# Kernel optimization log

Measured on AMD Instinct MI355X. Metric: run time of the kernel, lower is better.

Reference implementation:

```python
import math
import jax, jax.numpy as jnp
import numpy as np

DIM = 2048
NUM_HEADS = 16
HEAD_DIM = 128
SEQ = 2048
BATCH = 2
HIDDEN = 5632  # round_up(int(4*2048*2/3), 256)
EPS = 1e-6


def setup_inputs() -> dict:
    key = jax.random.key(0)
    ks = jax.random.split(key, 8)
    s = 0.02
    x = jax.random.normal(ks[0], (BATCH, SEQ, DIM), jnp.float32)
    wq = jax.random.normal(ks[1], (DIM, NUM_HEADS * HEAD_DIM), jnp.float32) * s
    wk = jax.random.normal(ks[2], (DIM, NUM_HEADS * HEAD_DIM), jnp.float32) * s
    wv = jax.random.normal(ks[3], (DIM, NUM_HEADS * HEAD_DIM), jnp.float32) * s
    wo = jax.random.normal(ks[4], (NUM_HEADS * HEAD_DIM, DIM), jnp.float32) * s
    w_mlp = jax.random.normal(ks[5], (HIDDEN, DIM), jnp.float32) * s
    v_mlp = jax.random.normal(ks[6], (HIDDEN, DIM), jnp.float32) * s
    w2_mlp = jax.random.normal(ks[7], (DIM, HIDDEN), jnp.float32) * s
    norm1_w = jnp.ones((DIM,), jnp.float32)
    norm2_w = jnp.ones((DIM,), jnp.float32)
    # RoPE tables: theta_i = 10000^{-2i/head_dim}, angle[p,i] = p * theta_i
    inv_freq = 1.0 / (10000.0 ** (np.arange(0, HEAD_DIM, 2, dtype=np.float32) / HEAD_DIM))
    angles = np.arange(SEQ, dtype=np.float32)[:, None] * inv_freq[None, :]  # [S, D/2]
    freqs_cos = jnp.asarray(np.cos(angles))
    freqs_sin = jnp.asarray(np.sin(angles))
    return {"x": x, "wq": wq, "wk": wk, "wv": wv, "wo": wo,
            "w_mlp": w_mlp, "v_mlp": v_mlp, "w2_mlp": w2_mlp,
            "norm1_w": norm1_w, "norm2_w": norm2_w,
            "freqs_cos": freqs_cos, "freqs_sin": freqs_sin}


def _rope(t, cos, sin):
    # t: [B,S,H,D] -> pairs, complex multiply by (cos + i sin)
    B, S, H, D = t.shape
    t = t.reshape(B, S, H, D // 2, 2)
    x0, x1 = t[..., 0], t[..., 1]
    c = cos[None, :S, None, :]
    s = sin[None, :S, None, :]
    o0 = x0 * c - x1 * s
    o1 = x0 * s + x1 * c
    return jnp.stack([o0, o1], axis=-1).reshape(B, S, H, D)


def _rmsnorm(x, w):
    x = x * jax.lax.rsqrt(jnp.mean(x * x, axis=-1, keepdims=True) + EPS)
    return w * x


def _attention(x, wq, wk, wv, wo, cos, sin):
    B, S, _ = x.shape
    q = (x @ wq).reshape(B, S, NUM_HEADS, HEAD_DIM)
    k = (x @ wk).reshape(B, S, NUM_HEADS, HEAD_DIM)
    v = (x @ wv).reshape(B, S, NUM_HEADS, HEAD_DIM)
    q = _rope(q, cos, sin)
    k = _rope(k, cos, sin)
    scores = jnp.einsum('bqhd,bkhd->bhqk', q, k) / math.sqrt(HEAD_DIM)
    causal = jnp.tril(jnp.ones((S, S), bool))
    scores = jnp.where(causal[None, None], scores, -jnp.inf)
    probs = jax.nn.softmax(scores.astype(jnp.float32), axis=-1)
    o = jnp.einsum('bhqk,bkhd->bqhd', probs, v).reshape(B, S, NUM_HEADS * HEAD_DIM)
    return o @ wo


def _mlp(x, w, v, w2):
    return (jax.nn.silu(x @ w.T) * (x @ v.T)) @ w2.T


def reference(x, wq, wk, wv, wo, w_mlp, v_mlp, w2_mlp, norm1_w, norm2_w, freqs_cos, freqs_sin):
    x = x + _attention(x, wq, wk, wv, wo, freqs_cos, freqs_sin)
    x = _rmsnorm(x, norm1_w)
    x = x + _mlp(x, w_mlp, v_mlp, w2_mlp)
    x = _rmsnorm(x, norm2_w)
    return x
```

## Files before the change

kernel.cpp:

```cpp
#include <hip/hip_runtime.h>

typedef unsigned short u16;
typedef unsigned int u32;
typedef float f32x4 __attribute__((ext_vector_type(4)));
typedef short bf16x8 __attribute__((ext_vector_type(8)));

#define DIM 2048
#define SEQ 2048
#define NHEAD 16
#define HDIM 128
#define BATCH 2
#define HIDDEN 5632
#define ROWS 4096

__device__ __forceinline__ float b2f(u16 h) { return __uint_as_float(((u32)h) << 16); }
__device__ __forceinline__ u16 f2b(float f) {
  u32 u = __float_as_uint(f);
  return (u16)((u + 0x7fffu + ((u >> 16) & 1u)) >> 16);
}

__global__ __launch_bounds__(256) void cvt_f2b(const float* __restrict__ in, u16* __restrict__ out, int n) {
  int i = (blockIdx.x * 256 + threadIdx.x) * 4;
  if (i < n) {
    float4 v = *(const float4*)(in + i);
    u32 p0 = (u32)f2b(v.x) | ((u32)f2b(v.y) << 16);
    u32 p1 = (u32)f2b(v.z) | ((u32)f2b(v.w) << 16);
    *(uint2*)(out + i) = make_uint2(p0, p1);
  }
}

__global__ __launch_bounds__(256) void cvtT(const float* __restrict__ in, u16* __restrict__ out,
                                            int Rr, int Cc) {
  __shared__ float t[32][33];
  int tx = threadIdx.x & 31, ty = threadIdx.x >> 5;
  int r0 = blockIdx.y * 32, c0 = blockIdx.x * 32;
#pragma unroll
  for (int rr = 0; rr < 4; ++rr)
    t[ty + rr * 8][tx] = in[(size_t)(r0 + ty + rr * 8) * Cc + c0 + tx];
  __syncthreads();
#pragma unroll
  for (int rr = 0; rr < 4; ++rr)
    out[(size_t)(c0 + ty + rr * 8) * Rr + r0 + tx] = f2b(t[tx][ty + rr * 8]);
}

__device__ __forceinline__ void stage_tile(u16* lds, const u16* __restrict__ g,
                                           int row0, int col0, int ld, int wave, int lane) {
#pragma unroll
  for (int j = 0; j < 2; ++j) {
    int i = wave * 2 + j;
    const u16* gp = g + (size_t)(row0 + i * 16 + (lane >> 2)) * ld + col0 + (lane & 3) * 8;
    __builtin_amdgcn_global_load_lds((const __attribute__((address_space(1))) void*)gp,
                                     (__attribute__((address_space(3))) void*)(lds + i * 512),
                                     16, 0, 0);
  }
}

template <int EPI>
__global__ __launch_bounds__(256) void gemm_bt(const u16* __restrict__ A, const u16* __restrict__ Bt,
                                               const void* R_, void* C_, int M, int N, int K) {
  __shared__ u16 lA[2][4096];
  __shared__ u16 lB[2][4096];
  const int tid = threadIdx.x, lane = tid & 63, wave = tid >> 6;
  const int wm = wave >> 1, wn = wave & 1;
  const int gx = gridDim.x;
  const int nwg = gx * gridDim.y;
  const int id = blockIdx.y * gx + blockIdx.x;
  const int cpx = nwg >> 3;
  const int sw = (id & 7) * cpx + (id >> 3);
  const int m0 = (sw / gx) * 128, n0 = (sw % gx) * 128;
  const int rl = lane & 15, g = lane >> 4;

  stage_tile(lA[0], A, m0, 0, K, wave, lane);
  stage_tile(lB[0], Bt, n0, 0, K, wave, lane);

  f32x4 acc[4][4];
#pragma unroll
  for (int a = 0; a < 4; ++a)
#pragma unroll
    for (int b = 0; b < 4; ++b) acc[a][b] = (f32x4){0.f, 0.f, 0.f, 0.f};

  __syncthreads();

  const int nk = K / 32;
  for (int kt = 0; kt < nk; ++kt) {
    const int cur = kt & 1;
    if (kt + 1 < nk) {
      stage_tile(lA[cur ^ 1], A, m0, (kt + 1) * 32, K, wave, lane);
      stage_tile(lB[cur ^ 1], Bt, n0, (kt + 1) * 32, K, wave, lane);
    }
    bf16x8 af[4], bfr[4];
#pragma unroll
    for (int mi = 0; mi < 4; ++mi)
      af[mi] = *reinterpret_cast<const bf16x8*>(&lA[cur][(wm * 64 + mi * 16 + rl) * 32 + g * 8]);
#pragma unroll
    for (int ni = 0; ni < 4; ++ni)
      bfr[ni] = *reinterpret_cast<const bf16x8*>(&lB[cur][(wn * 64 + ni * 16 + rl) * 32 + g * 8]);
#pragma unroll
    for (int mi = 0; mi < 4; ++mi)
#pragma unroll
      for (int ni = 0; ni < 4; ++ni)
        acc[mi][ni] = __builtin_amdgcn_mfma_f32_16x16x32_bf16(af[mi], bfr[ni], acc[mi][ni], 0, 0, 0);
    __syncthreads();
  }

#pragma unroll
  for (int mi = 0; mi < 4; ++mi)
#pragma unroll
    for (int ni = 0; ni < 4; ++ni)
#pragma unroll
      for (int j = 0; j < 4; ++j) {
        size_t row = m0 + wm * 64 + mi * 16 + g * 4 + j;
        size_t col = n0 + wn * 64 + ni * 16 + rl;
        size_t idx = row * N + col;
        float v = acc[mi][ni][j];
        if (EPI == 0) {
          ((u16*)C_)[idx] = f2b(v);
        } else if (EPI == 1) {
          ((float*)C_)[idx] = v + ((const float*)R_)[idx];
        } else if (EPI == 2) {
          float av = b2f(((const u16*)R_)[idx]);
          ((u16*)C_)[idx] = f2b(v * av / (1.f + __expf(-av)));
        } else if (EPI == 3) {
          ((float*)C_)[idx] = v + b2f(((const u16*)R_)[idx]);
        } else {
          size_t di = (col >> 11) * (size_t)(ROWS * (size_t)DIM) + row * DIM + (col & (DIM - 1));
          ((u16*)C_)[di] = f2b(v);
        }
      }
}

__global__ __launch_bounds__(256) void vtrans(const u16* __restrict__ V, u16* __restrict__ Vt) {
  __shared__ u16 t[32][33];
  int tx = threadIdx.x & 31, ty = threadIdx.x >> 5;
  int s0 = blockIdx.x * 32, d0 = blockIdx.y * 32;
  int bh = blockIdx.z, b = bh >> 4, h = bh & 15;
#pragma unroll
  for (int rr = 0; rr < 4; ++rr)
    t[ty + rr * 8][tx] = V[(size_t)(b * SEQ + s0 + ty + rr * 8) * DIM + h * HDIM + d0 + tx];
  __syncthreads();
#pragma unroll
  for (int rr = 0; rr < 4; ++rr)
    Vt[(size_t)(bh * HDIM + d0 + ty + rr * 8) * SEQ + s0 + tx] = t[tx][ty + rr * 8];
}

__global__ __launch_bounds__(256) void rope_kernel(u16* __restrict__ Q, u16* __restrict__ Kv,
                                                   const float* __restrict__ Cz, const float* __restrict__ Sz) {
  int t = blockIdx.x * 256 + threadIdx.x;
  int i = t & 63;
  int hh = (t >> 6) & 15;
  int row = t >> 10;
  int s = row & (SEQ - 1);
  float c = Cz[s * 64 + i], sn = Sz[s * 64 + i];
  size_t off = (size_t)row * DIM + hh * HDIM + 2 * i;
  const float sc = 0.08838834764831843f;

  u32 qp = *(const u32*)(Q + off);
  float q0 = b2f((u16)qp), q1 = b2f((u16)(qp >> 16));
  float o0 = (q0 * c - q1 * sn) * sc, o1 = (q0 * sn + q1 * c) * sc;
  *(u32*)(Q + off) = (u32)f2b(o0) | ((u32)f2b(o1) << 16);

  u32 kp = *(const u32*)(Kv + off);
  float k0 = b2f((u16)kp), k1 = b2f((u16)(kp >> 16));
  o0 = k0 * c - k1 * sn; o1 = k0 * sn + k1 * c;
  *(u32*)(Kv + off) = (u32)f2b(o0) | ((u32)f2b(o1) << 16);
}

__device__ __forceinline__ void attn_stage(u16* lk, u16* lv, const u16* __restrict__ Kg,
                                           const u16* __restrict__ Vg, int b, int h, int bh,
                                           int t, int w, int lane) {
  const int r4 = lane >> 2;
  const int gsw = (lane & 3) ^ (r4 & 3);
#pragma unroll
  for (int j = 0; j < 4; ++j) {
    const u16* gp = Kg + (size_t)(b * SEQ + t * 64 + j * 16 + r4) * DIM +
                    h * HDIM + w * 32 + gsw * 8;
    __builtin_amdgcn_global_load_lds((const __attribute__((address_space(1))) void*)gp,
                                     (__attribute__((address_space(3))) void*)(lk + w * 2048 + j * 512),
                                     16, 0, 0);
  }
#pragma unroll
  for (int j = 0; j < 4; ++j) {
    int id = w * 4 + j, kc2 = id >> 3, rg = id & 7;
    const u16* gp = Vg + (size_t)(bh * HDIM + rg * 16 + r4) * SEQ +
                    t * 64 + kc2 * 32 + gsw * 8;
    __builtin_amdgcn_global_load_lds((const __attribute__((address_space(1))) void*)gp,
                                     (__attribute__((address_space(3))) void*)(lv + kc2 * 4096 + rg * 512),
                                     16, 0, 0);
  }
}

__device__ __forceinline__ void attn_tile(const bf16x8* qf, float* m, float* l, f32x4* oacc,
                                          int qg0, int t, bool diag,
                                          const u16* lk, const u16* lv, u16 (*pl)[72],
                                          int rl, int g) {
  const int gx8 = (g ^ (rl & 3)) * 8;
  f32x4 s[4];
#pragma unroll
  for (int ct = 0; ct < 4; ++ct) s[ct] = (f32x4){0.f, 0.f, 0.f, 0.f};
#pragma unroll
  for (int ct = 0; ct < 4; ++ct)
#pragma unroll
    for (int kc = 0; kc < 4; ++kc) {
      bf16x8 kf = *reinterpret_cast<const bf16x8*>(&lk[kc * 2048 + (ct * 16 + rl) * 32 + gx8]);
      s[ct] = __builtin_amdgcn_mfma_f32_16x16x32_bf16(qf[kc], kf, s[ct], 0, 0, 0);
    }
  if (diag) {
#pragma unroll
    for (int ct = 0; ct < 4; ++ct) {
      int kg = t * 64 + ct * 16 + rl;
#pragma unroll
      for (int j = 0; j < 4; ++j)
        if (kg > qg0 + j) s[ct][j] = -1e30f;
    }
  }
  float mx[4], al[4];
#pragma unroll
  for (int j = 0; j < 4; ++j)
    mx[j] = fmaxf(fmaxf(s[0][j], s[1][j]), fmaxf(s[2][j], s[3][j]));
#pragma unroll
  for (int off = 1; off < 16; off <<= 1)
#pragma unroll
    for (int j = 0; j < 4; ++j) mx[j] = fmaxf(mx[j], __shfl_xor(mx[j], off));
#pragma unroll
  for (int j = 0; j < 4; ++j) {
    float mn = fmaxf(m[j], mx[j]);
    al[j] = __expf(m[j] - mn);
    m[j] = mn;
  }
  float rs[4] = {0.f, 0.f, 0.f, 0.f};
#pragma unroll
  for (int ct = 0; ct < 4; ++ct)
#pragma unroll
    for (int j = 0; j < 4; ++j) {
      float p = __expf(s[ct][j] - m[j]);
      s[ct][j] = p;
      rs[j] += p;
    }
#pragma unroll
  for (int off = 1; off < 16; off <<= 1)
#pragma unroll
    for (int j = 0; j < 4; ++j) rs[j] += __shfl_xor(rs[j], off);
#pragma unroll
  for (int j = 0; j < 4; ++j) l[j] = l[j] * al[j] + rs[j];
#pragma unroll
  for (int dt = 0; dt < 8; ++dt)
#pragma unroll
    for (int j = 0; j < 4; ++j) oacc[dt][j] *= al[j];

#pragma unroll
  for (int ct = 0; ct < 4; ++ct)
#pragma unroll
    for (int j = 0; j < 4; ++j) pl[g * 4 + j][ct * 16 + rl] = f2b(s[ct][j]);

  bf16x8 pa[2];
#pragma unroll
  for (int kc2 = 0; kc2 < 2; ++kc2)
    pa[kc2] = *reinterpret_cast<const bf16x8*>(&pl[rl][kc2 * 32 + g * 8]);

#pragma unroll
  for (int dt = 0; dt < 8; ++dt)
#pragma unroll
    for (int kc2 = 0; kc2 < 2; ++kc2) {
      bf16x8 vf = *reinterpret_cast<const bf16x8*>(&lv[kc2 * 4096 + (dt * 16 + rl) * 32 + gx8]);
      oacc[dt] = __builtin_amdgcn_mfma_f32_16x16x32_bf16(pa[kc2], vf, oacc[dt], 0, 0, 0);
    }
}

__global__ __launch_bounds__(256) void attn_kernel(const u16* __restrict__ Q, const u16* __restrict__ Kp,
                                                   const u16* __restrict__ Vt, u16* __restrict__ O) {
  const int lane = threadIdx.x & 63;
  const int w = threadIdx.x >> 6;
  const int id = blockIdx.y * 16 + blockIdx.x;
  const int sw = (id & 7) * 64 + (id >> 3);
  const int qa = sw & 15;
  const int qb = 31 - qa;
  const int bh = sw >> 4;
  const int b = bh >> 4, h = bh & 15;
  const int rl = lane & 15, g = lane >> 4;

  __shared__ u16 lK[2][8192];
  __shared__ u16 lV[2][8192];
  __shared__ u16 plds[4][16][72];

  const size_t qrowA = (size_t)b * SEQ + qa * 64 + w * 16;
  const size_t qrowB = (size_t)b * SEQ + qb * 64 + w * 16;
  bf16x8 qfA[4], qfB[4];
#pragma unroll
  for (int kc = 0; kc < 4; ++kc) {
    qfA[kc] = *reinterpret_cast<const bf16x8*>(Q + (qrowA + rl) * DIM + h * HDIM + kc * 32 + g * 8);
    qfB[kc] = *reinterpret_cast<const bf16x8*>(Q + (qrowB + rl) * DIM + h * HDIM + kc * 32 + g * 8);
  }

  float mA[4], lA_[4], mB[4], lB_[4];
  f32x4 oA[8], oB[8];
#pragma unroll
  for (int j = 0; j < 4; ++j) { mA[j] = -1e30f; lA_[j] = 0.f; mB[j] = -1e30f; lB_[j] = 0.f; }
#pragma unroll
  for (int dt = 0; dt < 8; ++dt) { oA[dt] = (f32x4){0.f, 0.f, 0.f, 0.f}; oB[dt] = (f32x4){0.f, 0.f, 0.f, 0.f}; }

  const int qg0A = qa * 64 + w * 16 + g * 4;
  const int qg0B = qb * 64 + w * 16 + g * 4;

  attn_stage(lK[0], lV[0], Kp, Vt, b, h, bh, 0, w, lane);

  int buf = 0;
  for (int t = 0; t <= qb; ++t) {
    if (t < qb) {
      attn_stage(lK[buf ^ 1], lV[buf ^ 1], Kp, Vt, b, h, bh, t + 1, w, lane);
      asm volatile("s_waitcnt vmcnt(8)" ::: "memory");
    } else {
      asm volatile("s_waitcnt vmcnt(0)" ::: "memory");
    }
    __builtin_amdgcn_s_barrier();
    __builtin_amdgcn_sched_barrier(0);
    attn_tile(qfB, mB, lB_, oB, qg0B, t, t == qb, lK[buf], lV[buf], plds[w], rl, g);
    if (t <= qa)
      attn_tile(qfA, mA, lA_, oA, qg0A, t, t == qa, lK[buf], lV[buf], plds[w], rl, g);
    asm volatile("s_waitcnt lgkmcnt(0)" ::: "memory");
    __builtin_amdgcn_sched_barrier(0);
    __builtin_amdgcn_s_barrier();
    buf ^= 1;
  }

  float invA[4], invB[4];
#pragma unroll
  for (int j = 0; j < 4; ++j) { invA[j] = 1.f / lA_[j]; invB[j] = 1.f / lB_[j]; }
#pragma unroll
  for (int dt = 0; dt < 8; ++dt)
#pragma unroll
    for (int j = 0; j < 4; ++j) {
      O[(qrowA + g * 4 + j) * DIM + h * HDIM + dt * 16 + rl] = f2b(oA[dt][j] * invA[j]);
      O[(qrowB + g * 4 + j) * DIM + h * HDIM + dt * 16 + rl] = f2b(oB[dt][j] * invB[j]);
    }
}

__global__ __launch_bounds__(256) void rmsnorm_to_bf16(const float* __restrict__ X, const float* __restrict__ W,
                                                       u16* __restrict__ O) {
  int row = blockIdx.x, tid = threadIdx.x;
  const float* xr = X + (size_t)row * DIM + tid * 8;
  float4 a = *(const float4*)xr;
  float4 bq = *(const float4*)(xr + 4);
  float v[8] = {a.x, a.y, a.z, a.w, bq.x, bq.y, bq.z, bq.w};
  float ss = 0.f;
#pragma unroll
  for (int j = 0; j < 8; ++j) ss += v[j] * v[j];
#pragma unroll
  for (int off = 32; off; off >>= 1) ss += __shfl_xor(ss, off);
  __shared__ float wss[4];
  int wave = tid >> 6, lane = tid & 63;
  if (lane == 0) wss[wave] = ss;
  __syncthreads();
  float r = rsqrtf((wss[0] + wss[1] + wss[2] + wss[3]) * (1.f / DIM) + 1e-6f);
  float4 wa = *(const float4*)(W + tid * 8);
  float4 wb = *(const float4*)(W + tid * 8 + 4);
  float wv[8] = {wa.x, wa.y, wa.z, wa.w, wb.x, wb.y, wb.z, wb.w};
  uint4 ou;
  ou.x = (u32)f2b(v[0] * r * wv[0]) | ((u32)f2b(v[1] * r * wv[1]) << 16);
  ou.y = (u32)f2b(v[2] * r * wv[2]) | ((u32)f2b(v[3] * r * wv[3]) << 16);
  ou.z = (u32)f2b(v[4] * r * wv[4]) | ((u32)f2b(v[5] * r * wv[5]) << 16);
  ou.w = (u32)f2b(v[6] * r * wv[6]) | ((u32)f2b(v[7] * r * wv[7]) << 16);
  *(uint4*)(O + (size_t)row * DIM + tid * 8) = ou;
}

__global__ __launch_bounds__(256) void rmsnorm_to_f32(const float* __restrict__ X, const float* __restrict__ W,
                                                      float* __restrict__ O) {
  int row = blockIdx.x, tid = threadIdx.x;
  const float* xr = X + (size_t)row * DIM + tid * 8;
  float4 a = *(const float4*)xr;
  float4 bq = *(const float4*)(xr + 4);
  float v[8] = {a.x, a.y, a.z, a.w, bq.x, bq.y, bq.z, bq.w};
  float ss = 0.f;
#pragma unroll
  for (int j = 0; j < 8; ++j) ss += v[j] * v[j];
#pragma unroll
  for (int off = 32; off; off >>= 1) ss += __shfl_xor(ss, off);
  __shared__ float wss[4];
  int wave = tid >> 6, lane = tid & 63;
  if (lane == 0) wss[wave] = ss;
  __syncthreads();
  float r = rsqrtf((wss[0] + wss[1] + wss[2] + wss[3]) * (1.f / DIM) + 1e-6f);
  float4 wa = *(const float4*)(W + tid * 8);
  float4 wb = *(const float4*)(W + tid * 8 + 4);
  float wv[8] = {wa.x, wa.y, wa.z, wa.w, wb.x, wb.y, wb.z, wb.w};
  float4 o0 = {v[0] * r * wv[0], v[1] * r * wv[1], v[2] * r * wv[2], v[3] * r * wv[3]};
  float4 o1 = {v[4] * r * wv[4], v[5] * r * wv[5], v[6] * r * wv[6], v[7] * r * wv[7]};
  *(float4*)(O + (size_t)row * DIM + tid * 8) = o0;
  *(float4*)(O + (size_t)row * DIM + tid * 8 + 4) = o1;
}

extern "C" void kernel_launch(void* const* d_in, const int* in_sizes, int n_in,
                              void* d_out, int out_size, void* d_ws, size_t ws_size,
                              hipStream_t stream) {
  const float* x     = (const float*)d_in[0];
  const float* wq    = (const float*)d_in[1];
  const float* wk    = (const float*)d_in[2];
  const float* wv    = (const float*)d_in[3];
  const float* wo    = (const float*)d_in[4];
  const float* w_mlp = (const float*)d_in[5];
  const float* v_mlp = (const float*)d_in[6];
  const float* w2    = (const float*)d_in[7];
  const float* n1w   = (const float*)d_in[8];
  const float* n2w   = (const float*)d_in[9];
  const float* fcos  = (const float*)d_in[10];
  const float* fsin  = (const float*)d_in[11];

  u16* ws = (u16*)d_ws;
  const size_t SZ = (size_t)ROWS * DIM;
  const size_t DD = (size_t)DIM * DIM;
  const size_t DH = (size_t)DIM * HIDDEN;

  u16* xb  = ws;
  u16* q   = ws + SZ;
  u16* k   = ws + 2 * SZ;
  u16* v   = ws + 3 * SZ;
  u16* vt  = ws + 4 * SZ;
  u16* hb  = ws + 5 * SZ;
  u16* W   = ws + 6 * SZ;
  u16* wqT = W;
  u16* wkT = W + DD;
  u16* wvT = W + 2 * DD;
  u16* woT = W + 3 * DD;
  u16* wmb = W;
  u16* vmb = W + DH;
  u16* w2b = W;
  float* x1f = (float*)ws;
  float* x2f = (float*)ws;
  u16* ba  = ws + 2 * SZ;

  dim3 blk(256);

  cvt_f2b<<<(int)(SZ / 4 / 256), blk, 0, stream>>>(x, xb, (int)SZ);
  dim3 gT(DIM / 32, DIM / 32);
  cvtT<<<gT, blk, 0, stream>>>(wq, wqT, DIM, DIM);
  cvtT<<<gT, blk, 0, stream>>>(wk, wkT, DIM, DIM);
  cvtT<<<gT, blk, 0, stream>>>(wv, wvT, DIM, DIM);
  cvtT<<<gT, blk, 0, stream>>>(wo, woT, DIM, DIM);

  dim3 gQKV(3 * DIM / 128, ROWS / 128);
  gemm_bt<4><<<gQKV, blk, 0, stream>>>(xb, W, nullptr, q, ROWS, 3 * DIM, DIM);

  cvt_f2b<<<(int)(DH / 4 / 256), blk, 0, stream>>>(w_mlp, wmb, (int)DH);

  rope_kernel<<<(ROWS * NHEAD * 64) / 256, blk, 0, stream>>>(q, k, fcos, fsin);
  vtrans<<<dim3(SEQ / 32, HDIM / 32, BATCH * NHEAD), blk, 0, stream>>>(v, vt);

  attn_kernel<<<dim3(16, BATCH * NHEAD), blk, 0, stream>>>(q, k, vt, v);

  dim3 gP(DIM / 128, ROWS / 128);
  gemm_bt<1><<<gP, blk, 0, stream>>>(v, woT, x, x1f, ROWS, DIM, DIM);

  cvt_f2b<<<(int)(DH / 4 / 256), blk, 0, stream>>>(v_mlp, vmb, (int)DH);

  rmsnorm_to_bf16<<<ROWS, blk, 0, stream>>>(x1f, n1w, hb);

  dim3 gM1(HIDDEN / 128, ROWS / 128);
  gemm_bt<0><<<gM1, blk, 0, stream>>>(hb, wmb, nullptr, ba, ROWS, HIDDEN, DIM);
  gemm_bt<2><<<gM1, blk, 0, stream>>>(hb, vmb, ba, ba, ROWS, HIDDEN, DIM);

  cvt_f2b<<<(int)(DH / 4 / 256), blk, 0, stream>>>(w2, w2b, (int)DH);

  gemm_bt<3><<<gP, blk, 0, stream>>>(ba, w2b, hb, x2f, ROWS, DIM, HIDDEN);
  rmsnorm_to_f32<<<ROWS, blk, 0, stream>>>(x2f, n2w, (float*)d_out);
}
```

Measured before the change: 842.7 us.

## Add 256x256 eight-wave pipelined GEMM for QKV and MLP up projections

Adds a new 512-thread GEMM kernel with 256x256 output tiles. It double-buffers LDS through direct global-to-LDS loads and interleaves the next tile's loads with MFMA phases, using explicit waitcnt, barriers and setprio. It also remaps block IDs in a swizzled order for L2 locality. The QKV and both MLP up-projection GEMMs now use it instead of the 128x128 kernel, aiming for more data reuse and better overlap of memory with compute. The cost is higher register and LDS pressure, and hand-tuned synchronization that is fragile.

```diff
diff --git a/kernel.cpp b/kernel.cpp
--- a/kernel.cpp
+++ b/kernel.cpp
@@ -129,6 +129,114 @@
       }
 }
 
+template <int EPI>
+__global__ __launch_bounds__(512, 2) void gemm8p(const u16* __restrict__ A, const u16* __restrict__ Bt,
+                                                 const void* R_, void* C_, int M, int N, int K) {
+  __shared__ u16 L[2][2][2][8192];
+  const int tid = threadIdx.x;
+  const int lane = tid & 63, wid = tid >> 6;
+  const int wr = wid >> 2, wc = wid & 3;
+  const int rl = lane & 15, g = lane >> 4;
+  const int s2 = ((rl >> 3) & 1) << 1;
+  const int gx = gridDim.x;
+  const int id = blockIdx.y * gx + blockIdx.x;
+  const int cpx = (gx * gridDim.y) >> 3;
+  const int sw = (id & 7) * cpx + (id >> 3);
+  const int m0 = (sw / gx) * 256, n0 = (sw % gx) * 256;
+  const int nk = K >> 6;
+
+  const int srow = tid >> 2;
+  const int sslot = (tid & 3) ^ (((tid >> 5) & 1) << 1);
+
+  auto SH = [&](int ks, int ab, int hf) {
+    const u16* src = ab ? Bt : A;
+    const u16* gp = src + (size_t)((ab ? n0 : m0) + hf * 128 + srow) * K + ks * 64 + sslot * 8;
+#pragma unroll
+    for (int kk = 0; kk < 2; ++kk)
+      __builtin_amdgcn_global_load_lds(
+          (const __attribute__((address_space(1))) void*)(gp + kk * 32),
+          (__attribute__((address_space(3))) void*)&L[ks & 1][ab][hf][kk * 4096 + wid * 512],
+          16, 0, 0);
+  };
+
+  f32x4 acc[8][4];
+#pragma unroll
+  for (int a = 0; a < 8; ++a)
+#pragma unroll
+    for (int b = 0; b < 4; ++b) acc[a][b] = (f32x4){0.f, 0.f, 0.f, 0.f};
+  bf16x8 bf[4][2];
+
+#define PHASE8(kst, q, STAGE, VMN)                                                              \
+  do {                                                                                          \
+    const int c_ = (kst) & 1;                                                                   \
+    if ((q) == 0) {                                                                             \
+      _Pragma("unroll") for (int ni = 0; ni < 4; ++ni)                                          \
+          _Pragma("unroll") for (int kk = 0; kk < 2; ++kk)                                      \
+              bf[ni][kk] = *(const bf16x8*)&L[c_][1][wc >> 1]                                   \
+                  [kk * 4096 + ((wc & 1) * 64 + ni * 16 + rl) * 32 + (g ^ s2) * 8];             \
+    }                                                                                           \
+    bf16x8 af[2][2];                                                                            \
+    _Pragma("unroll") for (int mm = 0; mm < 2; ++mm)                                            \
+        _Pragma("unroll") for (int kk = 0; kk < 2; ++kk)                                        \
+            af[mm][kk] = *(const bf16x8*)&L[c_][0][wr]                                          \
+                [kk * 4096 + (((q) * 2 + mm) * 16 + rl) * 32 + (g ^ s2) * 8];                   \
+    STAGE;                                                                                      \
+    __builtin_amdgcn_s_barrier();                                                               \
+    asm volatile("s_waitcnt lgkmcnt(0)" ::: "memory");                                          \
+    __builtin_amdgcn_sched_barrier(0);                                                          \
+    __builtin_amdgcn_s_setprio(1);                                                              \
+    _Pragma("unroll") for (int kk = 0; kk < 2; ++kk)                                            \
+        _Pragma("unroll") for (int mm = 0; mm < 2; ++mm)                                        \
+            _Pragma("unroll") for (int ni = 0; ni < 4; ++ni)                                    \
+                acc[(q) * 2 + mm][ni] = __builtin_amdgcn_mfma_f32_16x16x32_bf16(                \
+                    af[mm][kk], bf[ni][kk], acc[(q) * 2 + mm][ni], 0, 0, 0);                    \
+    __builtin_amdgcn_s_setprio(0);                                                              \
+    if ((VMN) == 4) asm volatile("s_waitcnt vmcnt(4)" ::: "memory");                            \
+    else if ((VMN) == 0) asm volatile("s_waitcnt vmcnt(0)" ::: "memory");                       \
+    __builtin_amdgcn_s_barrier();                                                               \
+  } while (0)
+
+  SH(0, 0, 0); SH(0, 0, 1); SH(0, 1, 0); SH(0, 1, 1); SH(1, 1, 0); SH(1, 1, 1);
+  asm volatile("s_waitcnt vmcnt(4)" ::: "memory");
+  __builtin_amdgcn_s_barrier();
+
+  const int nk2 = nk >> 1;
+  for (int i = 0; i < nk2; ++i) {
+    const int k0 = 2 * i, k1 = 2 * i + 1;
+    const bool st2 = (k0 + 2) < nk, st3 = (k0 + 3) < nk;
+    PHASE8(k0, 0, SH(k1, 0, 0), -1);
+    PHASE8(k0, 1, SH(k1, 0, 1), -1);
+    PHASE8(k0, 2, if (st2) SH(k0 + 2, 1, 0), -1);
+    PHASE8(k0, 3, if (st2) SH(k0 + 2, 1, 1), st2 ? 4 : 0);
+    PHASE8(k1, 0, if (st2) SH(k0 + 2, 0, 0), -1);
+    PHASE8(k1, 1, if (st2) SH(k0 + 2, 0, 1), -1);
+    PHASE8(k1, 2, if (st3) SH(k0 + 3, 1, 0), -1);
+    PHASE8(k1, 3, if (st3) SH(k0 + 3, 1, 1), st2 ? 4 : 0);
+  }
+#undef PHASE8
+
+#pragma unroll
+  for (int mi = 0; mi < 8; ++mi)
+#pragma unroll
+    for (int ni = 0; ni < 4; ++ni)
+#pragma unroll
+      for (int j = 0; j < 4; ++j) {
+        size_t row = m0 + wr * 128 + mi * 16 + g * 4 + j;
+        size_t col = n0 + wc * 64 + ni * 16 + rl;
+        size_t idx = row * N + col;
+        float v = acc[mi][ni][j];
+        if (EPI == 0) {
+          ((u16*)C_)[idx] = f2b(v);
+        } else if (EPI == 2) {
+          float av = b2f(((const u16*)R_)[idx]);
+          ((u16*)C_)[idx] = f2b(v * av / (1.f + __expf(-av)));
+        } else {
+          size_t di = (col >> 11) * (size_t)(ROWS * (size_t)DIM) + row * DIM + (col & (DIM - 1));
+          ((u16*)C_)[di] = f2b(v);
+        }
+      }
+}
+
 __global__ __launch_bounds__(256) void vtrans(const u16* __restrict__ V, u16* __restrict__ Vt) {
   __shared__ u16 t[32][33];
   int tx = threadIdx.x & 31, ty = threadIdx.x >> 5;
@@ -428,6 +536,7 @@
   u16* ba  = ws + 2 * SZ;
 
   dim3 blk(256);
+  dim3 blk8(512);
 
   cvt_f2b<<<(int)(SZ / 4 / 256), blk, 0, stream>>>(x, xb, (int)SZ);
   dim3 gT(DIM / 32, DIM / 32);
@@ -436,8 +545,8 @@
   cvtT<<<gT, blk, 0, stream>>>(wv, wvT, DIM, DIM);
   cvtT<<<gT, blk, 0, stream>>>(wo, woT, DIM, DIM);
 
-  dim3 gQKV(3 * DIM / 128, ROWS / 128);
-  gemm_bt<4><<<gQKV, blk, 0, stream>>>(xb, W, nullptr, q, ROWS, 3 * DIM, DIM);
+  dim3 gQKV(3 * DIM / 256, ROWS / 256);
+  gemm8p<4><<<gQKV, blk8, 0, stream>>>(xb, W, nullptr, q, ROWS, 3 * DIM, DIM);
 
   cvt_f2b<<<(int)(DH / 4 / 256), blk, 0, stream>>>(w_mlp, wmb, (int)DH);
 
@@ -453,9 +562,9 @@
 
   rmsnorm_to_bf16<<<ROWS, blk, 0, stream>>>(x1f, n1w, hb);
 
-  dim3 gM1(HIDDEN / 128, ROWS / 128);
-  gemm_bt<0><<<gM1, blk, 0, stream>>>(hb, wmb, nullptr, ba, ROWS, HIDDEN, DIM);
-  gemm_bt<2><<<gM1, blk, 0, stream>>>(hb, vmb, ba, ba, ROWS, HIDDEN, DIM);
+  dim3 gM8(HIDDEN / 256, ROWS / 256);
+  gemm8p<0><<<gM8, blk8, 0, stream>>>(hb, wmb, nullptr, ba, ROWS, HIDDEN, DIM);
+  gemm8p<2><<<gM8, blk8, 0, stream>>>(hb, vmb, ba, ba, ROWS, HIDDEN, DIM);
 
   cvt_f2b<<<(int)(DH / 4 / 256), blk, 0, stream>>>(w2, w2b, (int)DH);
 
```

Measured after the change: 868.0 us. 1.03x slower.
